# Kernel optimization log

Measured on AMD Instinct MI355X. Metric: run time of the kernel, lower is better.

## Reference

```python
import jax, jax.numpy as jnp
import numpy as np

B, S, H, D = 8, 16, 32, 64
HID = H * D
PAST = 4096


def setup_inputs() -> dict:
    key = jax.random.key(0)
    ks = jax.random.split(key, 7)
    sc = 0.02
    return {
        "hidden_states": jax.random.normal(ks[0], (B, S, HID), jnp.float32),
        "past_k": jax.random.normal(ks[1], (B, H, PAST, D), jnp.float32),
        "past_v": jax.random.normal(ks[2], (B, H, PAST, D), jnp.float32),
        "wq": jax.random.normal(ks[3], (HID, HID), jnp.float32) * sc,
        "wk": jax.random.normal(ks[4], (HID, HID), jnp.float32) * sc,
        "wv": jax.random.normal(ks[5], (HID, HID), jnp.float32) * sc,
        "wo": jax.random.normal(ks[6], (HID, HID), jnp.float32) * sc,
    }


def reference(hidden_states, past_k, past_v, wq, wk, wv, wo):
    b, s, _ = hidden_states.shape
    # QKV projections (torch Linear: x @ W.T), split into heads -> [B,H,S,D]
    q = (hidden_states @ wq.T).reshape(b, s, H, D).transpose(0, 2, 1, 3)
    k = (hidden_states @ wk.T).reshape(b, s, H, D).transpose(0, 2, 1, 3)
    v = (hidden_states @ wv.T).reshape(b, s, H, D).transpose(0, 2, 1, 3)
    # KV-cache concat: [B,H,past+S,D]
    k = jnp.concatenate([past_k, k], axis=2)
    v = jnp.concatenate([past_v, v], axis=2)
    scale = 1.0 / jnp.sqrt(jnp.asarray(D, hidden_states.dtype))
    # scores [B,H,S,T]
    scores = jnp.einsum("bhsd,bhtd->bhst", q, k) * scale
    probs = jax.nn.softmax(scores, axis=-1)
    out = jnp.einsum("bhst,bhtd->bhsd", probs, v)
    out = out.transpose(0, 2, 1, 3).reshape(b, s, HID)
    return out @ wo.T
```

## Files before the change

kernel.cpp:

```cpp
#include <hip/hip_runtime.h>
#include <hip/hip_bf16.h>
#include <stdint.h>

#define HID 2048
#define NH  32
#define HD  64
#define NB  8
#define NS  16
#define PAST 4096

#define QSCALE 0.18033688011112042591f

typedef __attribute__((ext_vector_type(8))) short short8;
typedef __attribute__((ext_vector_type(4))) short short4v;
typedef __attribute__((ext_vector_type(4))) float f32x4;

#define MFMA(a, b, c) __builtin_amdgcn_mfma_f32_16x16x32_bf16((a), (b), (c), 0, 0, 0)

#define PART_STRIDE 1088
#define NSPLIT 4
#define MATSZ (128 * HID)
#define VPAD 68

static __device__ __forceinline__ short f2bf(float f) {
    __hip_bfloat16 h = __float2bfloat16(f);
    return *reinterpret_cast<short*>(&h);
}

static __device__ __forceinline__ short8 pack8(float4 a, float4 b) {
    short8 r;
    r[0] = f2bf(a.x); r[1] = f2bf(a.y); r[2] = f2bf(a.z); r[3] = f2bf(a.w);
    r[4] = f2bf(b.x); r[5] = f2bf(b.y); r[6] = f2bf(b.z); r[7] = f2bf(b.w);
    return r;
}

static __device__ __forceinline__ short8 pack8s(float4 a, float4 b, float s) {
    short8 r;
    r[0] = f2bf(a.x * s); r[1] = f2bf(a.y * s); r[2] = f2bf(a.z * s); r[3] = f2bf(a.w * s);
    r[4] = f2bf(b.x * s); r[5] = f2bf(b.y * s); r[6] = f2bf(b.z * s); r[7] = f2bf(b.w * s);
    return r;
}

__global__ __launch_bounds__(256) void cvt_kernel(const float* __restrict__ in,
                                                  short* __restrict__ out) {
    int i = (blockIdx.x * 256 + threadIdx.x) * 4;
    float4 v = *reinterpret_cast<const float4*>(in + i);
    short4v o;
    o[0] = f2bf(v.x); o[1] = f2bf(v.y); o[2] = f2bf(v.z); o[3] = f2bf(v.w);
    *reinterpret_cast<short4v*>(out + i) = o;
}

__global__ __launch_bounds__(128) void proj_kernel(
        const short* __restrict__ X,
        const float* __restrict__ W0, const float* __restrict__ W1,
        const float* __restrict__ W2,
        float* __restrict__ Yp) {
    int mat   = blockIdx.x >> 9;
    int rest  = blockIdx.x & 511;
    int strip = rest >> 2, ks = rest & 3;
    int nbase = strip * 16;
    int k0    = ks * 512;
    const float* W = (mat == 0) ? W0 : (mat == 1) ? W1 : W2;
    float* Y = Yp + (size_t)(mat * 4 + ks) * MATSZ;

    int lane = threadIdx.x & 63;
    int wave = threadIdx.x >> 6;
    int lr = lane & 15, g = lane >> 4;

    f32x4 acc0 = {0.f, 0.f, 0.f, 0.f};
    f32x4 acc1 = {0.f, 0.f, 0.f, 0.f};
    f32x4 acc2 = {0.f, 0.f, 0.f, 0.f};
    f32x4 acc3 = {0.f, 0.f, 0.f, 0.f};

    const short* xr = X + (size_t)(wave * 64 + lr) * HID + g * 8 + k0;
    const float* wr = W + (size_t)(nbase + lr) * HID + g * 8 + k0;

    #pragma unroll 4
    for (int kc = 0; kc < 512; kc += 32) {
        float4 w0 = *reinterpret_cast<const float4*>(wr + kc);
        float4 w1 = *reinterpret_cast<const float4*>(wr + kc + 4);
        short8 bb = pack8(w0, w1);
        short8 a0 = *reinterpret_cast<const short8*>(xr + kc);
        short8 a1 = *reinterpret_cast<const short8*>(xr + (size_t)16 * HID + kc);
        short8 a2 = *reinterpret_cast<const short8*>(xr + (size_t)32 * HID + kc);
        short8 a3 = *reinterpret_cast<const short8*>(xr + (size_t)48 * HID + kc);
        acc0 = MFMA(a0, bb, acc0);
        acc1 = MFMA(a1, bb, acc1);
        acc2 = MFMA(a2, bb, acc2);
        acc3 = MFMA(a3, bb, acc3);
    }
    #define STACC(accv, f) do { \
        Y[(size_t)(wave * 64 + (f) * 16 + (g << 2) + 0) * HID + nbase + lr] = accv[0]; \
        Y[(size_t)(wave * 64 + (f) * 16 + (g << 2) + 1) * HID + nbase + lr] = accv[1]; \
        Y[(size_t)(wave * 64 + (f) * 16 + (g << 2) + 2) * HID + nbase + lr] = accv[2]; \
        Y[(size_t)(wave * 64 + (f) * 16 + (g << 2) + 3) * HID + nbase + lr] = accv[3]; \
    } while (0)
    STACC(acc0, 0); STACC(acc1, 1); STACC(acc2, 2); STACC(acc3, 3);
    #undef STACC
}

__global__ __launch_bounds__(256) void merge4_kernel(
        const float* __restrict__ Yp,
        float* __restrict__ Y0, float* __restrict__ Y1, float* __restrict__ Y2) {
    int mat = blockIdx.x >> 8;
    int blk = blockIdx.x & 255;
    float* Y = (mat == 0) ? Y0 : (mat == 1) ? Y1 : Y2;
    const float* P = Yp + (size_t)mat * 4 * MATSZ;
    int idx = blk * 1024 + threadIdx.x * 4;
    float4 a = *reinterpret_cast<const float4*>(P + idx);
    float4 b = *reinterpret_cast<const float4*>(P + MATSZ + idx);
    float4 c = *reinterpret_cast<const float4*>(P + 2 * MATSZ + idx);
    float4 d = *reinterpret_cast<const float4*>(P + 3 * MATSZ + idx);
    float4 s;
    s.x = a.x + b.x + c.x + d.x;
    s.y = a.y + b.y + c.y + d.y;
    s.z = a.z + b.z + c.z + d.z;
    s.w = a.w + b.w + c.w + d.w;
    *reinterpret_cast<float4*>(Y + idx) = s;
}

__global__ __launch_bounds__(256, 4) void attn_kernel(
        const float* __restrict__ q,
        const float* __restrict__ knew, const float* __restrict__ vnew,
        const float* __restrict__ pastK, const float* __restrict__ pastV,
        float* __restrict__ parts) {
    __shared__ __align__(16) float lds_v[4][2][16 * VPAD];
    __shared__ float s_m[4][16];
    __shared__ float s_l[4][16];

    int bid = blockIdx.x;
    int bh = bid >> 2, split = bid & 3;
    int b = bh >> 5, h = bh & 31;
    int wave = threadIdx.x >> 6, lane = threadIdx.x & 63;
    int lq = lane & 15, g = lane >> 4;
    int vrow = lane >> 4;
    int vcol = (lane & 15) * 4;

    const float* qp = q + (size_t)(b * NS + lq) * HID + h * HD + g * 8;
    short8 qf0, qf1;
    {
        float4 a0 = *reinterpret_cast<const float4*>(qp);
        float4 a1 = *reinterpret_cast<const float4*>(qp + 4);
        float4 a2 = *reinterpret_cast<const float4*>(qp + 32);
        float4 a3 = *reinterpret_cast<const float4*>(qp + 36);
        qf0 = pack8s(a0, a1, QSCALE);
        qf1 = pack8s(a2, a3, QSCALE);
    }

    f32x4 o0 = {0.f, 0.f, 0.f, 0.f};
    f32x4 o1 = {0.f, 0.f, 0.f, 0.f};
    f32x4 o2 = {0.f, 0.f, 0.f, 0.f};
    f32x4 o3 = {0.f, 0.f, 0.f, 0.f};
    float m = -__builtin_inff(), lsum = 0.0f;

    const float* ksplit = pastK + (size_t)bh * PAST * HD + (size_t)split * 1024 * HD;
    const float* vsplit = pastV + (size_t)bh * PAST * HD + (size_t)split * 1024 * HD;

    #define ISSUE_K(T, A, Bv, C, D) do { \
        const float* kr_ = ksplit + (size_t)((T) * 64 + wave * 16 + lq) * HD + (g << 3); \
        A  = *reinterpret_cast<const float4*>(kr_); \
        Bv = *reinterpret_cast<const float4*>(kr_ + 4); \
        C  = *reinterpret_cast<const float4*>(kr_ + 32); \
        D  = *reinterpret_cast<const float4*>(kr_ + 36); \
    } while (0)

    #define ISSUE_V(T, V0, V1, V2, V3) do { \
        const float* vr_ = vsplit + (size_t)((T) * 64 + wave * 16) * HD; \
        V0 = *reinterpret_cast<const float4*>(vr_ + (0 * 4 + vrow) * HD + vcol); \
        V1 = *reinterpret_cast<const float4*>(vr_ + (1 * 4 + vrow) * HD + vcol); \
        V2 = *reinterpret_cast<const float4*>(vr_ + (2 * 4 + vrow) * HD + vcol); \
        V3 = *reinterpret_cast<const float4*>(vr_ + (3 * 4 + vrow) * HD + vcol); \
    } while (0)

    #define DSW(V0, V1, V2, V3, BUF) do { \
        float* ds_ = &lds_v[wave][BUF][0]; \
        *reinterpret_cast<float4*>(ds_ + (0 * 4 + vrow) * VPAD + vcol) = V0; \
        *reinterpret_cast<float4*>(ds_ + (1 * 4 + vrow) * VPAD + vcol) = V1; \
        *reinterpret_cast<float4*>(ds_ + (2 * 4 + vrow) * VPAD + vcol) = V2; \
        *reinterpret_cast<float4*>(ds_ + (3 * 4 + vrow) * VPAD + vcol) = V3; \
    } while (0)

    #define QKSM(A, Bv, C, D, PF) do { \
        short8 af0 = pack8(A, Bv); \
        short8 af1 = pack8(C, D); \
        f32x4 sv = {0.f, 0.f, 0.f, 0.f}; \
        sv = MFMA(af0, qf0, sv); \
        sv = MFMA(af1, qf1, sv); \
        float tmax = fmaxf(fmaxf(sv[0], sv[1]), fmaxf(sv[2], sv[3])); \
        tmax = fmaxf(tmax, __shfl_xor(tmax, 16)); \
        tmax = fmaxf(tmax, __shfl_xor(tmax, 32)); \
        float mn = fmaxf(m, tmax); \
        float alpha = exp2f(m - mn); \
        float e0 = exp2f(sv[0] - mn); \
        float e1 = exp2f(sv[1] - mn); \
        float e2 = exp2f(sv[2] - mn); \
        float e3 = exp2f(sv[3] - mn); \
        float rsum = e0 + e1 + e2 + e3; \
        rsum += __shfl_xor(rsum, 16); \
        rsum += __shfl_xor(rsum, 32); \
        lsum = lsum * alpha + rsum; \
        m = mn; \
        o0 *= alpha; o1 *= alpha; o2 *= alpha; o3 *= alpha; \
        PF[0] = f2bf(e0); PF[1] = f2bf(e1); PF[2] = f2bf(e2); PF[3] = f2bf(e3); \
        PF[4] = 0; PF[5] = 0; PF[6] = 0; PF[7] = 0; \
    } while (0)

    #define PV(BUF, PF) do { \
        const float* vc = &lds_v[wave][BUF][(g << 2) * VPAD]; \
        short8 vf; \
        vf[4] = 0; vf[5] = 0; vf[6] = 0; vf[7] = 0; \
        vf[0] = f2bf(vc[0 * VPAD + lq]);      vf[1] = f2bf(vc[1 * VPAD + lq]); \
        vf[2] = f2bf(vc[2 * VPAD + lq]);      vf[3] = f2bf(vc[3 * VPAD + lq]); \
        o0 = MFMA(vf, PF, o0); \
        vf[0] = f2bf(vc[0 * VPAD + 16 + lq]); vf[1] = f2bf(vc[1 * VPAD + 16 + lq]); \
        vf[2] = f2bf(vc[2 * VPAD + 16 + lq]); vf[3] = f2bf(vc[3 * VPAD + 16 + lq]); \
        o1 = MFMA(vf, PF, o1); \
        vf[0] = f2bf(vc[0 * VPAD + 32 + lq]); vf[1] = f2bf(vc[1 * VPAD + 32 + lq]); \
        vf[2] = f2bf(vc[2 * VPAD + 32 + lq]); vf[3] = f2bf(vc[3 * VPAD + 32 + lq]); \
        o2 = MFMA(vf, PF, o2); \
        vf[0] = f2bf(vc[0 * VPAD + 48 + lq]); vf[1] = f2bf(vc[1 * VPAD + 48 + lq]); \
        vf[2] = f2bf(vc[2 * VPAD + 48 + lq]); vf[3] = f2bf(vc[3 * VPAD + 48 + lq]); \
        o3 = MFMA(vf, PF, o3); \
    } while (0)

    float4 kA0, kA1, kA2, kA3, kB0, kB1, kB2, kB3;
    float4 vA0, vA1, vA2, vA3, vB0, vB1, vB2, vB3;

    ISSUE_V(0, vA0, vA1, vA2, vA3);
    ISSUE_K(0, kA0, kA1, kA2, kA3);
    DSW(vA0, vA1, vA2, vA3, 0);

    #pragma unroll 1
    for (int tt = 0; tt < 8; ++tt) {
        ISSUE_V(2 * tt + 1, vB0, vB1, vB2, vB3);
        ISSUE_K(2 * tt + 1, kB0, kB1, kB2, kB3);
        short8 pfE;
        QKSM(kA0, kA1, kA2, kA3, pfE);
        PV(0, pfE);
        DSW(vB0, vB1, vB2, vB3, 1);
        if (tt < 7) {
            ISSUE_V(2 * tt + 2, vA0, vA1, vA2, vA3);
            ISSUE_K(2 * tt + 2, kA0, kA1, kA2, kA3);
        }
        short8 pfO;
        QKSM(kB0, kB1, kB2, kB3, pfO);
        PV(1, pfO);
        if (tt < 7) DSW(vA0, vA1, vA2, vA3, 0);
    }
    #undef PV
    #undef QKSM
    #undef DSW
    #undef ISSUE_V
    #undef ISSUE_K

    if (split == 0 && wave == 0) {
        const float* kr = knew + (size_t)(b * NS + lq) * HID + h * HD + g * 8;
        float4 ka = *reinterpret_cast<const float4*>(kr);
        float4 kb2 = *reinterpret_cast<const float4*>(kr + 4);
        float4 kc2 = *reinterpret_cast<const float4*>(kr + 32);
        float4 kd2 = *reinterpret_cast<const float4*>(kr + 36);
        short8 af0 = pack8(ka, kb2);
        short8 af1 = pack8(kc2, kd2);
        f32x4 sv = {0.f, 0.f, 0.f, 0.f};
        sv = MFMA(af0, qf0, sv);
        sv = MFMA(af1, qf1, sv);

        float tmax = fmaxf(fmaxf(sv[0], sv[1]), fmaxf(sv[2], sv[3]));
        tmax = fmaxf(tmax, __shfl_xor(tmax, 16));
        tmax = fmaxf(tmax, __shfl_xor(tmax, 32));
        float mn = fmaxf(m, tmax);
        float alpha = exp2f(m - mn);
        float e0 = exp2f(sv[0] - mn);
        float e1 = exp2f(sv[1] - mn);
        float e2 = exp2f(sv[2] - mn);
        float e3 = exp2f(sv[3] - mn);
        float rsum = e0 + e1 + e2 + e3;
        rsum += __shfl_xor(rsum, 16);
        rsum += __shfl_xor(rsum, 32);
        lsum = lsum * alpha + rsum;
        m = mn;
        o0 *= alpha; o1 *= alpha; o2 *= alpha; o3 *= alpha;

        short8 pfT;
        pfT[0] = f2bf(e0); pfT[1] = f2bf(e1); pfT[2] = f2bf(e2); pfT[3] = f2bf(e3);
        pfT[4] = 0; pfT[5] = 0; pfT[6] = 0; pfT[7] = 0;

        const float* vt2 = vnew + (size_t)(b * NS) * HID + h * HD;
        #define LOADVT(dst, dcol) do { \
            dst[0] = f2bf(vt2[(size_t)((g << 2) + 0) * HID + (dcol)]); \
            dst[1] = f2bf(vt2[(size_t)((g << 2) + 1) * HID + (dcol)]); \
            dst[2] = f2bf(vt2[(size_t)((g << 2) + 2) * HID + (dcol)]); \
            dst[3] = f2bf(vt2[(size_t)((g << 2) + 3) * HID + (dcol)]); \
            dst[4] = 0; dst[5] = 0; dst[6] = 0; dst[7] = 0; \
        } while (0)
        short8 vv0, vv1, vv2, vv3;
        LOADVT(vv0, lq); LOADVT(vv1, 16 + lq); LOADVT(vv2, 32 + lq); LOADVT(vv3, 48 + lq);
        #undef LOADVT
        o0 = MFMA(vv0, pfT, o0);
        o1 = MFMA(vv1, pfT, o1);
        o2 = MFMA(vv2, pfT, o2);
        o3 = MFMA(vv3, pfT, o3);
    }

    float* so_w = &lds_v[wave][0][0];
    #define STO(ov, dt) do { \
        so_w[lq * 64 + (dt) * 16 + (g << 2) + 0] = ov[0]; \
        so_w[lq * 64 + (dt) * 16 + (g << 2) + 1] = ov[1]; \
        so_w[lq * 64 + (dt) * 16 + (g << 2) + 2] = ov[2]; \
        so_w[lq * 64 + (dt) * 16 + (g << 2) + 3] = ov[3]; \
    } while (0)
    STO(o0, 0); STO(o1, 1); STO(o2, 2); STO(o3, 3);
    #undef STO
    if (g == 0) { s_m[wave][lq] = m; s_l[wave][lq] = lsum; }
    __syncthreads();

    if (wave == 0) {
        float M = fmaxf(fmaxf(s_m[0][lq], s_m[1][lq]), fmaxf(s_m[2][lq], s_m[3][lq]));
        float aw0 = exp2f(s_m[0][lq] - M);
        float aw1 = exp2f(s_m[1][lq] - M);
        float aw2 = exp2f(s_m[2][lq] - M);
        float aw3 = exp2f(s_m[3][lq] - M);
        float L = aw0 * s_l[0][lq] + aw1 * s_l[1][lq] + aw2 * s_l[2][lq] + aw3 * s_l[3][lq];
        const float* so0 = &lds_v[0][0][0];
        const float* so1 = &lds_v[1][0][0];
        const float* so2 = &lds_v[2][0][0];
        const float* so3 = &lds_v[3][0][0];
        float* pbase = parts + (size_t)bid * PART_STRIDE;
        if (g == 0) { pbase[lq] = M; pbase[16 + lq] = L; }
        for (int dd = 0; dd < 16; ++dd) {
            int di = g * 16 + dd;
            float v = aw0 * so0[lq * 64 + di] + aw1 * so1[lq * 64 + di] +
                      aw2 * so2[lq * 64 + di] + aw3 * so3[lq * 64 + di];
            pbase[32 + lq * 64 + di] = v;
        }
    }
}

__global__ __launch_bounds__(256) void merge_kernel(const float* __restrict__ parts,
                                                    short* __restrict__ attnb) {
    int bh = blockIdx.x;
    int tid = threadIdx.x;
    int qi = tid >> 4, ds = (tid & 15) * 4;
    const float* p0 = parts + (size_t)(bh * NSPLIT) * PART_STRIDE;
    const float* p1 = p0 + PART_STRIDE;
    const float* p2 = p1 + PART_STRIDE;
    const float* p3 = p2 + PART_STRIDE;
    float m0 = p0[qi], m1 = p1[qi], m2 = p2[qi], m3 = p3[qi];
    float M = fmaxf(fmaxf(m0, m1), fmaxf(m2, m3));
    float a0 = exp2f(m0 - M), a1 = exp2f(m1 - M), a2 = exp2f(m2 - M), a3 = exp2f(m3 - M);
    float inv = 1.0f / (a0 * p0[16 + qi] + a1 * p1[16 + qi] +
                        a2 * p2[16 + qi] + a3 * p3[16 + qi]);
    int b = bh >> 5, h = bh & 31;
    int base = 32 + qi * 64 + ds;
    float v0 = (a0 * p0[base + 0] + a1 * p1[base + 0] + a2 * p2[base + 0] + a3 * p3[base + 0]) * inv;
    float v1 = (a0 * p0[base + 1] + a1 * p1[base + 1] + a2 * p2[base + 1] + a3 * p3[base + 1]) * inv;
    float v2 = (a0 * p0[base + 2] + a1 * p1[base + 2] + a2 * p2[base + 2] + a3 * p3[base + 2]) * inv;
    float v3 = (a0 * p0[base + 3] + a1 * p1[base + 3] + a2 * p2[base + 3] + a3 * p3[base + 3]) * inv;
    short4v o;
    o[0] = f2bf(v0); o[1] = f2bf(v1); o[2] = f2bf(v2); o[3] = f2bf(v3);
    *reinterpret_cast<short4v*>(attnb + (size_t)(b * NS + qi) * HID + h * HD + ds) = o;
}

extern "C" void kernel_launch(void* const* d_in, const int* in_sizes, int n_in,
                              void* d_out, int out_size, void* d_ws, size_t ws_size,
                              hipStream_t stream) {
    const float* hs     = (const float*)d_in[0];
    const float* past_k = (const float*)d_in[1];
    const float* past_v = (const float*)d_in[2];
    const float* wq     = (const float*)d_in[3];
    const float* wk     = (const float*)d_in[4];
    const float* wv     = (const float*)d_in[5];
    const float* wo     = (const float*)d_in[6];
    float* out = (float*)d_out;

    float* qb    = (float*)d_ws;
    float* kn    = qb + MATSZ;
    float* vn    = kn + MATSZ;
    short* hsb   = (short*)(vn + MATSZ);
    short* attnb = hsb + MATSZ;
    float* parts = (float*)(attnb + MATSZ);
    float* qkvp  = parts + 1024 * PART_STRIDE;
    float* op    = qkvp + 3 * 4 * MATSZ;

    cvt_kernel<<<256, 256, 0, stream>>>(hs, hsb);
    proj_kernel<<<1536, 128, 0, stream>>>(hsb, wq, wk, wv, qkvp);
    merge4_kernel<<<768, 256, 0, stream>>>(qkvp, qb, kn, vn);
    attn_kernel<<<256 * NSPLIT, 256, 0, stream>>>(qb, kn, vn, past_k, past_v, parts);
    merge_kernel<<<256, 256, 0, stream>>>(parts, attnb);
    proj_kernel<<<512, 128, 0, stream>>>(attnb, wo, wo, wo, op);
    merge4_kernel<<<256, 256, 0, stream>>>(op, out, out, out);
}
```

Before: 180.1 us.

## Split KV over eight blocks, stage V as bf16 in LDS, reorder prefetch

```diff
diff --git a/kernel.cpp b/kernel.cpp
--- a/kernel.cpp
+++ b/kernel.cpp
@@ -18,9 +18,10 @@
 #define MFMA(a, b, c) __builtin_amdgcn_mfma_f32_16x16x32_bf16((a), (b), (c), 0, 0, 0)
 
 #define PART_STRIDE 1088
-#define NSPLIT 4
+#define NSPLIT 8
 #define MATSZ (128 * HID)
-#define VPAD 68
+#define VP 68
+#define WSLAB 4352
 
 static __device__ __forceinline__ short f2bf(float f) {
     __hip_bfloat16 h = __float2bfloat16(f);
@@ -31,6 +32,12 @@
     short8 r;
     r[0] = f2bf(a.x); r[1] = f2bf(a.y); r[2] = f2bf(a.z); r[3] = f2bf(a.w);
     r[4] = f2bf(b.x); r[5] = f2bf(b.y); r[6] = f2bf(b.z); r[7] = f2bf(b.w);
+    return r;
+}
+
+static __device__ __forceinline__ short4v pack4(float4 a) {
+    short4v r;
+    r[0] = f2bf(a.x); r[1] = f2bf(a.y); r[2] = f2bf(a.z); r[3] = f2bf(a.w);
     return r;
 }
 
@@ -124,17 +131,20 @@
         const float* __restrict__ knew, const float* __restrict__ vnew,
         const float* __restrict__ pastK, const float* __restrict__ pastV,
         float* __restrict__ parts) {
-    __shared__ __align__(16) float lds_v[4][2][16 * VPAD];
+    __shared__ __align__(16) unsigned char lds_raw[4 * WSLAB];
     __shared__ float s_m[4][16];
     __shared__ float s_l[4][16];
 
     int bid = blockIdx.x;
-    int bh = bid >> 2, split = bid & 3;
+    int bh = bid >> 3, split = bid & 7;
     int b = bh >> 5, h = bh & 31;
     int wave = threadIdx.x >> 6, lane = threadIdx.x & 63;
     int lq = lane & 15, g = lane >> 4;
     int vrow = lane >> 4;
     int vcol = (lane & 15) * 4;
+
+    unsigned short* vbuf0 = (unsigned short*)(lds_raw + wave * WSLAB);
+    unsigned short* vbuf1 = vbuf0 + 16 * VP;
 
     const float* qp = q + (size_t)(b * NS + lq) * HID + h * HD + g * 8;
     short8 qf0, qf1;
@@ -153,8 +163,8 @@
     f32x4 o3 = {0.f, 0.f, 0.f, 0.f};
     float m = -__builtin_inff(), lsum = 0.0f;
 
-    const float* ksplit = pastK + (size_t)bh * PAST * HD + (size_t)split * 1024 * HD;
-    const float* vsplit = pastV + (size_t)bh * PAST * HD + (size_t)split * 1024 * HD;
+    const float* ksplit = pastK + (size_t)bh * PAST * HD + (size_t)split * 512 * HD;
+    const float* vsplit = pastV + (size_t)bh * PAST * HD + (size_t)split * 512 * HD;
 
     #define ISSUE_K(T, A, Bv, C, D) do { \
         const float* kr_ = ksplit + (size_t)((T) * 64 + wave * 16 + lq) * HD + (g << 3); \
@@ -172,12 +182,12 @@
         V3 = *reinterpret_cast<const float4*>(vr_ + (3 * 4 + vrow) * HD + vcol); \
     } while (0)
 
-    #define DSW(V0, V1, V2, V3, BUF) do { \
-        float* ds_ = &lds_v[wave][BUF][0]; \
-        *reinterpret_cast<float4*>(ds_ + (0 * 4 + vrow) * VPAD + vcol) = V0; \
-        *reinterpret_cast<float4*>(ds_ + (1 * 4 + vrow) * VPAD + vcol) = V1; \
-        *reinterpret_cast<float4*>(ds_ + (2 * 4 + vrow) * VPAD + vcol) = V2; \
-        *reinterpret_cast<float4*>(ds_ + (3 * 4 + vrow) * VPAD + vcol) = V3; \
+    #define DSW(V0, V1, V2, V3, BUFP) do { \
+        unsigned short* ds_ = (BUFP); \
+        *reinterpret_cast<short4v*>(ds_ + (0 * 4 + vrow) * VP + vcol) = pack4(V0); \
+        *reinterpret_cast<short4v*>(ds_ + (1 * 4 + vrow) * VP + vcol) = pack4(V1); \
+        *reinterpret_cast<short4v*>(ds_ + (2 * 4 + vrow) * VP + vcol) = pack4(V2); \
+        *reinterpret_cast<short4v*>(ds_ + (3 * 4 + vrow) * VP + vcol) = pack4(V3); \
     } while (0)
 
     #define QKSM(A, Bv, C, D, PF) do { \
@@ -205,21 +215,21 @@
         PF[4] = 0; PF[5] = 0; PF[6] = 0; PF[7] = 0; \
     } while (0)
 
-    #define PV(BUF, PF) do { \
-        const float* vc = &lds_v[wave][BUF][(g << 2) * VPAD]; \
+    #define PV(BUFP, PF) do { \
+        const unsigned short* vc = (BUFP) + (g << 2) * VP; \
         short8 vf; \
         vf[4] = 0; vf[5] = 0; vf[6] = 0; vf[7] = 0; \
-        vf[0] = f2bf(vc[0 * VPAD + lq]);      vf[1] = f2bf(vc[1 * VPAD + lq]); \
-        vf[2] = f2bf(vc[2 * VPAD + lq]);      vf[3] = f2bf(vc[3 * VPAD + lq]); \
+        vf[0] = (short)vc[0 * VP + lq];      vf[1] = (short)vc[1 * VP + lq]; \
+        vf[2] = (short)vc[2 * VP + lq];      vf[3] = (short)vc[3 * VP + lq]; \
         o0 = MFMA(vf, PF, o0); \
-        vf[0] = f2bf(vc[0 * VPAD + 16 + lq]); vf[1] = f2bf(vc[1 * VPAD + 16 + lq]); \
-        vf[2] = f2bf(vc[2 * VPAD + 16 + lq]); vf[3] = f2bf(vc[3 * VPAD + 16 + lq]); \
+        vf[0] = (short)vc[0 * VP + 16 + lq]; vf[1] = (short)vc[1 * VP + 16 + lq]; \
+        vf[2] = (short)vc[2 * VP + 16 + lq]; vf[3] = (short)vc[3 * VP + 16 + lq]; \
         o1 = MFMA(vf, PF, o1); \
-        vf[0] = f2bf(vc[0 * VPAD + 32 + lq]); vf[1] = f2bf(vc[1 * VPAD + 32 + lq]); \
-        vf[2] = f2bf(vc[2 * VPAD + 32 + lq]); vf[3] = f2bf(vc[3 * VPAD + 32 + lq]); \
+        vf[0] = (short)vc[0 * VP + 32 + lq]; vf[1] = (short)vc[1 * VP + 32 + lq]; \
+        vf[2] = (short)vc[2 * VP + 32 + lq]; vf[3] = (short)vc[3 * VP + 32 + lq]; \
         o2 = MFMA(vf, PF, o2); \
-        vf[0] = f2bf(vc[0 * VPAD + 48 + lq]); vf[1] = f2bf(vc[1 * VPAD + 48 + lq]); \
-        vf[2] = f2bf(vc[2 * VPAD + 48 + lq]); vf[3] = f2bf(vc[3 * VPAD + 48 + lq]); \
+        vf[0] = (short)vc[0 * VP + 48 + lq]; vf[1] = (short)vc[1 * VP + 48 + lq]; \
+        vf[2] = (short)vc[2 * VP + 48 + lq]; vf[3] = (short)vc[3 * VP + 48 + lq]; \
         o3 = MFMA(vf, PF, o3); \
     } while (0)
 
@@ -228,24 +238,28 @@
 
     ISSUE_V(0, vA0, vA1, vA2, vA3);
     ISSUE_K(0, kA0, kA1, kA2, kA3);
-    DSW(vA0, vA1, vA2, vA3, 0);
+    DSW(vA0, vA1, vA2, vA3, vbuf0);
+    ISSUE_V(1, vB0, vB1, vB2, vB3);
+    ISSUE_K(1, kB0, kB1, kB2, kB3);
 
     #pragma unroll 1
-    for (int tt = 0; tt < 8; ++tt) {
-        ISSUE_V(2 * tt + 1, vB0, vB1, vB2, vB3);
-        ISSUE_K(2 * tt + 1, kB0, kB1, kB2, kB3);
+    for (int tt = 0; tt < 4; ++tt) {
         short8 pfE;
         QKSM(kA0, kA1, kA2, kA3, pfE);
-        PV(0, pfE);
-        DSW(vB0, vB1, vB2, vB3, 1);
-        if (tt < 7) {
+        DSW(vB0, vB1, vB2, vB3, vbuf1);
+        if (tt < 3) {
             ISSUE_V(2 * tt + 2, vA0, vA1, vA2, vA3);
             ISSUE_K(2 * tt + 2, kA0, kA1, kA2, kA3);
         }
+        PV(vbuf0, pfE);
         short8 pfO;
         QKSM(kB0, kB1, kB2, kB3, pfO);
-        PV(1, pfO);
-        if (tt < 7) DSW(vA0, vA1, vA2, vA3, 0);
+        if (tt < 3) {
+            DSW(vA0, vA1, vA2, vA3, vbuf0);
+            ISSUE_V(2 * tt + 3, vB0, vB1, vB2, vB3);
+            ISSUE_K(2 * tt + 3, kB0, kB1, kB2, kB3);
+        }
+        PV(vbuf1, pfO);
     }
     #undef PV
     #undef QKSM
@@ -302,7 +316,7 @@
         o3 = MFMA(vv3, pfT, o3);
     }
 
-    float* so_w = &lds_v[wave][0][0];
+    float* so_w = (float*)(lds_raw + wave * WSLAB);
     #define STO(ov, dt) do { \
         so_w[lq * 64 + (dt) * 16 + (g << 2) + 0] = ov[0]; \
         so_w[lq * 64 + (dt) * 16 + (g << 2) + 1] = ov[1]; \
@@ -321,10 +335,10 @@
         float aw2 = exp2f(s_m[2][lq] - M);
         float aw3 = exp2f(s_m[3][lq] - M);
         float L = aw0 * s_l[0][lq] + aw1 * s_l[1][lq] + aw2 * s_l[2][lq] + aw3 * s_l[3][lq];
-        const float* so0 = &lds_v[0][0][0];
-        const float* so1 = &lds_v[1][0][0];
-        const float* so2 = &lds_v[2][0][0];
-        const float* so3 = &lds_v[3][0][0];
+        const float* so0 = (const float*)(lds_raw + 0 * WSLAB);
+        const float* so1 = (const float*)(lds_raw + 1 * WSLAB);
+        const float* so2 = (const float*)(lds_raw + 2 * WSLAB);
+        const float* so3 = (const float*)(lds_raw + 3 * WSLAB);
         float* pbase = parts + (size_t)bid * PART_STRIDE;
         if (g == 0) { pbase[lq] = M; pbase[16 + lq] = L; }
         for (int dd = 0; dd < 16; ++dd) {
@@ -341,23 +355,39 @@
     int bh = blockIdx.x;
     int tid = threadIdx.x;
     int qi = tid >> 4, ds = (tid & 15) * 4;
-    const float* p0 = parts + (size_t)(bh * NSPLIT) * PART_STRIDE;
-    const float* p1 = p0 + PART_STRIDE;
-    const float* p2 = p1 + PART_STRIDE;
-    const float* p3 = p2 + PART_STRIDE;
-    float m0 = p0[qi], m1 = p1[qi], m2 = p2[qi], m3 = p3[qi];
-    float M = fmaxf(fmaxf(m0, m1), fmaxf(m2, m3));
-    float a0 = exp2f(m0 - M), a1 = exp2f(m1 - M), a2 = exp2f(m2 - M), a3 = exp2f(m3 - M);
-    float inv = 1.0f / (a0 * p0[16 + qi] + a1 * p1[16 + qi] +
-                        a2 * p2[16 + qi] + a3 * p3[16 + qi]);
+    const float* pb0 = parts + (size_t)(bh * NSPLIT) * PART_STRIDE;
+
+    float M = -__builtin_inff();
+    #pragma unroll
+    for (int i = 0; i < NSPLIT; ++i)
+        M = fmaxf(M, pb0[(size_t)i * PART_STRIDE + qi]);
+
+    float aw0, aw1, aw2, aw3, aw4, aw5, aw6, aw7;
+    float L = 0.f;
+    #define AW(i, awv) do { \
+        awv = exp2f(pb0[(size_t)(i) * PART_STRIDE + qi] - M); \
+        L += awv * pb0[(size_t)(i) * PART_STRIDE + 16 + qi]; \
+    } while (0)
+    AW(0, aw0); AW(1, aw1); AW(2, aw2); AW(3, aw3);
+    AW(4, aw4); AW(5, aw5); AW(6, aw6); AW(7, aw7);
+    #undef AW
+    float inv = 1.0f / L;
+
     int b = bh >> 5, h = bh & 31;
     int base = 32 + qi * 64 + ds;
-    float v0 = (a0 * p0[base + 0] + a1 * p1[base + 0] + a2 * p2[base + 0] + a3 * p3[base + 0]) * inv;
-    float v1 = (a0 * p0[base + 1] + a1 * p1[base + 1] + a2 * p2[base + 1] + a3 * p3[base + 1]) * inv;
-    float v2 = (a0 * p0[base + 2] + a1 * p1[base + 2] + a2 * p2[base + 2] + a3 * p3[base + 2]) * inv;
-    float v3 = (a0 * p0[base + 3] + a1 * p1[base + 3] + a2 * p2[base + 3] + a3 * p3[base + 3]) * inv;
     short4v o;
-    o[0] = f2bf(v0); o[1] = f2bf(v1); o[2] = f2bf(v2); o[3] = f2bf(v3);
+    #pragma unroll
+    for (int r = 0; r < 4; ++r) {
+        float v = aw0 * pb0[(size_t)0 * PART_STRIDE + base + r]
+                + aw1 * pb0[(size_t)1 * PART_STRIDE + base + r]
+                + aw2 * pb0[(size_t)2 * PART_STRIDE + base + r]
+                + aw3 * pb0[(size_t)3 * PART_STRIDE + base + r]
+                + aw4 * pb0[(size_t)4 * PART_STRIDE + base + r]
+                + aw5 * pb0[(size_t)5 * PART_STRIDE + base + r]
+                + aw6 * pb0[(size_t)6 * PART_STRIDE + base + r]
+                + aw7 * pb0[(size_t)7 * PART_STRIDE + base + r];
+        o[r] = f2bf(v * inv);
+    }
     *reinterpret_cast<short4v*>(attnb + (size_t)(b * NS + qi) * HID + h * HD + ds) = o;
 }
 
@@ -379,7 +409,7 @@
     short* hsb   = (short*)(vn + MATSZ);
     short* attnb = hsb + MATSZ;
     float* parts = (float*)(attnb + MATSZ);
-    float* qkvp  = parts + 1024 * PART_STRIDE;
+    float* qkvp  = parts + 2048 * PART_STRIDE;
     float* op    = qkvp + 3 * 4 * MATSZ;
 
     cvt_kernel<<<256, 256, 0, stream>>>(hs, hsb);
```

After: 180.7 us. About the same (+0.4%).
